# Performance work log

Measured on AMD Instinct MI355X. Metric: run time of the kernel, lower is better.

## Reference

```python
import jax, jax.numpy as jnp
import numpy as np

N_CELLS = 50000
HID = 64
DEG = 16
K_NODES = 4  # nodes per cell; cell i owns nodes [4i, 4i+4)
SP = 3


def setup_inputs() -> dict:
    key = jax.random.key(0)
    ks = jax.random.split(key, 12)
    s = 1.0 / np.sqrt(HID)
    inp = {
        'features': jax.random.normal(ks[0], (N_CELLS, HID), jnp.float32),
        'positions': jax.random.normal(ks[1], (K_NODES * N_CELLS, SP), jnp.float32),
        'neighbors': jax.random.randint(ks[2], (N_CELLS, DEG), 0, N_CELLS, jnp.int32),
        # message MLP: Linear(2H+1 -> H), SiLU, Linear(H -> H)
        'W1': jax.random.normal(ks[3], (2 * HID + 1, HID), jnp.float32) * s,
        'b1': jnp.zeros((HID,), jnp.float32),
        'W2': jax.random.normal(ks[4], (HID, HID), jnp.float32) * s,
        'b2': jnp.zeros((HID,), jnp.float32),
        # update MLP: Linear(H + H -> H), SiLU, Linear(H -> H)
        'Wu1': jax.random.normal(ks[5], (2 * HID, HID), jnp.float32) * s,
        'bu1': jnp.zeros((HID,), jnp.float32),
        'Wu2': jax.random.normal(ks[6], (HID, HID), jnp.float32) * s,
        'bu2': jnp.zeros((HID,), jnp.float32),
    }
    return inp


def reference(features, positions, neighbors, W1, b1, W2, b2, Wu1, bu1, Wu2, bu2):
    N, H = features.shape
    # centroid of each cell's owned nodes (cell i -> nodes [K*i, K*i+K))
    cent = positions.reshape(N, K_NODES, SP).mean(axis=1)          # [N, sp]
    fj = features[neighbors]                                       # [N, D, H]
    cj = cent[neighbors]                                           # [N, D, sp]
    # centroid-distance geometric invariant per (cell, neighbor) pair
    geom = jnp.linalg.norm(cent[:, None, :] - cj, axis=-1, keepdims=True)  # [N, D, 1]
    fi = jnp.broadcast_to(features[:, None, :], fj.shape)          # [N, D, H]
    x = jnp.concatenate([fi, fj, geom], axis=-1)                   # [N, D, 2H+1]
    h = jax.nn.silu(x @ W1 + b1) @ W2 + b2                         # [N, D, H]
    msg = h.mean(axis=1)                                           # mean over neighbors
    u = jnp.concatenate([features, msg], axis=-1)                  # [N, 2H]
    upd = jax.nn.silu(u @ Wu1 + bu1) @ Wu2 + bu2
    updated_features = features + upd
    return updated_features, positions
```

## Files before the change

kernel.cpp:

```cpp
#include <hip/hip_runtime.h>


#define DEG 16

typedef __attribute__((ext_vector_type(8))) short short8;
typedef __attribute__((ext_vector_type(4))) float f32x4;
typedef uint2 uint2_a __attribute__((may_alias));
typedef uint4 uint4_a __attribute__((may_alias));

union HbRd { uint4_a u; short8 s; };
union Frag { short8 s; uint4 u; };

__device__ __forceinline__ unsigned f2bf(float f) {
  unsigned u = __float_as_uint(f);
  return (u + 0x7FFFu + ((u >> 16) & 1u)) >> 16;
}
__device__ __forceinline__ float bf2f(unsigned bits16) {
  return __uint_as_float(bits16 << 16);
}
__device__ __forceinline__ float silu(float h) {
  return h / (1.f + __expf(-h));
}

__global__ __launch_bounds__(256) void aux_kernel(
    const float* __restrict__ pos,
    const float* __restrict__ W1, const float* __restrict__ W2,
    const float* __restrict__ Wu1, const float* __restrict__ Wu2,
    float* __restrict__ outpos,
    unsigned short* __restrict__ w1pq, unsigned short* __restrict__ w2t,
    unsigned short* __restrict__ wu1t, unsigned short* __restrict__ wu2b)
{
  int t = blockIdx.x * 256 + threadIdx.x;
  if (t < 150000) {
    ((float4*)outpos)[t] = ((const float4*)pos)[t];
  } else if (t < 174576) {
    const int r = t - 150000;
    if (r < 8192) {
      const int j = r & 7, l = (r >> 3) & 15, q = (r >> 7) & 3;
      const int f = r >> 9, kk = f & 1, mt = f >> 1;
      const int k = kk * 32 + q * 8 + j;
      const int m = mt * 16 + l;
      w1pq[r] = (unsigned short)f2bf(
          (m < 64) ? W1[k * 64 + m] : W1[(k + 64) * 64 + (m - 64)]);
    } else if (r < 12288) {
      const int s = r - 8192;
      const int j = s & 7, l = (s >> 3) & 15, q = (s >> 7) & 3;
      const int f = s >> 9, kk = f & 1, mt = f >> 1;
      const int k = kk * 32 + q * 8 + j;
      w2t[s] = (unsigned short)f2bf(W2[k * 64 + mt * 16 + l]);
    } else if (r < 20480) {
      const int s = r - 12288;
      const int j = s & 7, l = (s >> 3) & 15, q = (s >> 7) & 3;
      const int f = s >> 9, kk = f & 3, mt = f >> 2;
      const int k = kk * 32 + q * 8 + j;
      wu1t[s] = (unsigned short)f2bf(Wu1[k * 64 + mt * 16 + l]);
    } else {
      const int s = r - 20480;
      const int j = s & 7, l = (s >> 3) & 15, q = (s >> 7) & 3;
      const int f = s >> 9, kk = f & 1, nt = f >> 1;
      const int k = kk * 32 + q * 8 + j;
      wu2b[s] = (unsigned short)f2bf(Wu2[k * 64 + nt * 16 + l]);
    }
  }
}

__global__ __launch_bounds__(256) void prep_pq_kernel(
    const float* __restrict__ feat, const float* __restrict__ pos,
    const unsigned short* __restrict__ w1pq,
    unsigned short* __restrict__ featb, float* __restrict__ cent4,
    unsigned short* __restrict__ Pb, unsigned short* __restrict__ Qb)
{
  const int lane = threadIdx.x & 63;
  const int wid  = threadIdx.x >> 6;
  const int quad = lane >> 4;
  const int l15  = lane & 15;

  const int tile = blockIdx.x * 4 + wid;
  const bool act = (tile < 3125);
  const int  tt  = act ? tile : 3124;
  const int  cr  = tt * 16 + l15;

  short8 xf[2];
  #pragma unroll
  for (int kk = 0; kk < 2; ++kk) {
    const float4 f0 = *(const float4*)(feat + cr * 64 + kk * 32 + quad * 8);
    const float4 f1 = *(const float4*)(feat + cr * 64 + kk * 32 + quad * 8 + 4);
    Frag v;
    v.s[0] = (short)f2bf(f0.x); v.s[1] = (short)f2bf(f0.y);
    v.s[2] = (short)f2bf(f0.z); v.s[3] = (short)f2bf(f0.w);
    v.s[4] = (short)f2bf(f1.x); v.s[5] = (short)f2bf(f1.y);
    v.s[6] = (short)f2bf(f1.z); v.s[7] = (short)f2bf(f1.w);
    xf[kk] = v.s;
    if (act) *(uint4*)(featb + cr * 64 + kk * 32 + quad * 8) = v.u;
  }

  if (act && lane < 16) {
    const float4* pp = (const float4*)(pos + 12 * cr);
    const float4 a = pp[0], b = pp[1], c = pp[2];
    float4 o;
    o.x = (a.x + a.w + b.z + c.y) * 0.25f;
    o.y = (a.y + b.x + b.w + c.z) * 0.25f;
    o.z = (a.z + b.y + c.x + c.w) * 0.25f;
    o.w = 0.f;
    ((float4*)cent4)[cr] = o;
  }

  short8 wf[8][2];
  #pragma unroll
  for (int mt = 0; mt < 8; ++mt)
    #pragma unroll
    for (int kk = 0; kk < 2; ++kk)
      wf[mt][kk] = *(const short8*)(w1pq + (((mt * 2 + kk) * 4 + quad) << 7) + l15 * 8);

  f32x4 acc[8] = {};
  #pragma unroll
  for (int kk = 0; kk < 2; ++kk)
    #pragma unroll
    for (int mt = 0; mt < 8; ++mt)
      acc[mt] = __builtin_amdgcn_mfma_f32_16x16x32_bf16(wf[mt][kk], xf[kk], acc[mt], 0, 0, 0);

  if (act) {
    #pragma unroll
    for (int mt = 0; mt < 8; ++mt) {
      uint2 pk;
      pk.x = f2bf(acc[mt][0]) | (f2bf(acc[mt][1]) << 16);
      pk.y = f2bf(acc[mt][2]) | (f2bf(acc[mt][3]) << 16);
      unsigned short* dst = (mt < 4)
          ? Pb + cr * 64 + mt * 16 + quad * 4
          : Qb + cr * 64 + (mt - 4) * 16 + quad * 4;
      *(uint2*)dst = pk;
    }
  }
}

__global__ __launch_bounds__(256) void gather_kernel(
    const unsigned short* __restrict__ Pb,
    const unsigned short* __restrict__ Qb,
    const float4* __restrict__ cent4,
    const int* __restrict__ nbr,
    const float* __restrict__ b1, const float* __restrict__ W1,
    unsigned short* __restrict__ sB)
{
  const int lane = threadIdx.x & 63;
  const int wid  = threadIdx.x >> 6;
  const int quad = lane >> 4;
  const int l15  = lane & 15;
  const int c4   = l15 * 4;

  const f32x4 b1c = *(const f32x4*)(b1 + c4);
  const f32x4 wlc = *(const f32x4*)(W1 + 8192 + c4);

  for (int c = blockIdx.x * 4 + wid; c < 50000; c += 12500) {
    int nj = 0; float g = 0.f;
    if (lane < 16) {
      nj = nbr[c * DEG + lane];
      const float4 ci = cent4[c];
      const float4 cj = cent4[nj];
      const float dx = ci.x - cj.x, dy = ci.y - cj.y, dz = ci.z - cj.z;
      g = sqrtf(dx * dx + dy * dy + dz * dz);
    }

    const uint2 pv = *(const uint2*)(Pb + c * 64 + c4);
    float pc[4];
    pc[0] = bf2f(pv.x & 0xFFFFu) + b1c[0];
    pc[1] = bf2f(pv.x >> 16)     + b1c[1];
    pc[2] = bf2f(pv.y & 0xFFFFu) + b1c[2];
    pc[3] = bf2f(pv.y >> 16)     + b1c[3];

    float acc0 = 0.f, acc1 = 0.f, acc2 = 0.f, acc3 = 0.f;
    #pragma unroll
    for (int dd = 0; dd < 4; ++dd) {
      const int   d  = quad + dd * 4;
      const float gd = __shfl(g, d);
      const int   nd = __shfl(nj, d);
      const uint2 qv = *(const uint2*)(Qb + nd * 64 + c4);
      acc0 += silu(pc[0] + bf2f(qv.x & 0xFFFFu) + gd * wlc[0]);
      acc1 += silu(pc[1] + bf2f(qv.x >> 16)     + gd * wlc[1]);
      acc2 += silu(pc[2] + bf2f(qv.y & 0xFFFFu) + gd * wlc[2]);
      acc3 += silu(pc[3] + bf2f(qv.y >> 16)     + gd * wlc[3]);
    }
    acc0 += __shfl_xor(acc0, 16); acc0 += __shfl_xor(acc0, 32);
    acc1 += __shfl_xor(acc1, 16); acc1 += __shfl_xor(acc1, 32);
    acc2 += __shfl_xor(acc2, 16); acc2 += __shfl_xor(acc2, 32);
    acc3 += __shfl_xor(acc3, 16); acc3 += __shfl_xor(acc3, 32);

    if (lane < 16) {
      uint2 pk;
      pk.x = f2bf(acc0 * 0.0625f) | (f2bf(acc1 * 0.0625f) << 16);
      pk.y = f2bf(acc2 * 0.0625f) | (f2bf(acc3 * 0.0625f) << 16);
      *(uint2*)(sB + c * 64 + c4) = pk;
    }
  }
}

__global__ __launch_bounds__(256) void tail_kernel(
    const unsigned short* __restrict__ featb,
    const unsigned short* __restrict__ sB,
    const float* __restrict__ feat,
    const unsigned short* __restrict__ w2t,
    const unsigned short* __restrict__ wu1t,
    const unsigned short* __restrict__ wu2b,
    const float* __restrict__ b2, const float* __restrict__ bu1,
    const float* __restrict__ bu2,
    float* __restrict__ outf)
{
  __shared__ uint4 smem[4 * 288];
  const int lane = threadIdx.x & 63;
  const int wid  = threadIdx.x >> 6;
  const int quad = lane >> 4;
  const int l15  = lane & 15;
  char* Msg = (char*)(smem + wid * 288);
  char* Hb  = Msg + 2304;

  short8 w2f[4][2];
  #pragma unroll
  for (int mt = 0; mt < 4; ++mt)
    #pragma unroll
    for (int kk = 0; kk < 2; ++kk)
      w2f[mt][kk] = *(const short8*)(w2t + (((mt * 2 + kk) * 4 + quad) << 7) + l15 * 8);
  short8 wu1f[4][4];
  #pragma unroll
  for (int mt = 0; mt < 4; ++mt)
    #pragma unroll
    for (int kk = 0; kk < 4; ++kk)
      wu1f[mt][kk] = *(const short8*)(wu1t + (((mt * 4 + kk) * 4 + quad) << 7) + l15 * 8);
  short8 wu2f[4][2];
  #pragma unroll
  for (int nt = 0; nt < 4; ++nt)
    #pragma unroll
    for (int kk = 0; kk < 2; ++kk)
      wu2f[nt][kk] = *(const short8*)(wu2b + (((nt * 2 + kk) * 4 + quad) << 7) + l15 * 8);

  f32x4 b2f[4], bu1f[4];
  #pragma unroll
  for (int mt = 0; mt < 4; ++mt) {
    b2f[mt]  = *(const f32x4*)(b2  + mt * 16 + quad * 4);
    bu1f[mt] = *(const f32x4*)(bu1 + mt * 16 + quad * 4);
  }
  float bu2v[4];
  #pragma unroll
  for (int nt = 0; nt < 4; ++nt) bu2v[nt] = bu2[nt * 16 + l15];

  const int tile = blockIdx.x * 4 + wid;
  const bool act = (tile < 3125);
  const int  tt  = act ? tile : 3124;
  const int  cr  = tt * 16 + l15;

  f32x4 accm[4] = {};
  #pragma unroll
  for (int kk = 0; kk < 2; ++kk) {
    const short8 bf = *(const short8*)(sB + cr * 64 + kk * 32 + quad * 8);
    #pragma unroll
    for (int mt = 0; mt < 4; ++mt)
      accm[mt] = __builtin_amdgcn_mfma_f32_16x16x32_bf16(w2f[mt][kk], bf, accm[mt], 0, 0, 0);
  }
  #pragma unroll
  for (int mt = 0; mt < 4; ++mt) {
    uint2 pk;
    pk.x = f2bf(accm[mt][0] + b2f[mt][0]) | (f2bf(accm[mt][1] + b2f[mt][1]) << 16);
    pk.y = f2bf(accm[mt][2] + b2f[mt][2]) | (f2bf(accm[mt][3] + b2f[mt][3]) << 16);
    *(uint2_a*)(Msg + l15 * 144 + mt * 32 + quad * 8) = pk;
  }
  __threadfence_block();

  f32x4 accu[4] = {};
  #pragma unroll
  for (int kk = 0; kk < 4; ++kk) {
    short8 bf;
    if (kk < 2) {
      bf = *(const short8*)(featb + cr * 64 + kk * 32 + quad * 8);
    } else {
      HbRd t; t.u = *(const uint4_a*)(Msg + l15 * 144 + (kk - 2) * 64 + quad * 16);
      bf = t.s;
    }
    #pragma unroll
    for (int mt = 0; mt < 4; ++mt)
      accu[mt] = __builtin_amdgcn_mfma_f32_16x16x32_bf16(wu1f[mt][kk], bf, accu[mt], 0, 0, 0);
  }
  #pragma unroll
  for (int mt = 0; mt < 4; ++mt) {
    float sv[4];
    #pragma unroll
    for (int rg = 0; rg < 4; ++rg)
      sv[rg] = silu(accu[mt][rg] + bu1f[mt][rg]);
    uint2 pk;
    pk.x = f2bf(sv[0]) | (f2bf(sv[1]) << 16);
    pk.y = f2bf(sv[2]) | (f2bf(sv[3]) << 16);
    *(uint2_a*)(Hb + l15 * 144 + mt * 32 + quad * 8) = pk;
  }
  __threadfence_block();

  f32x4 acc2[4] = {};
  #pragma unroll
  for (int kk = 0; kk < 2; ++kk) {
    HbRd t; t.u = *(const uint4_a*)(Hb + l15 * 144 + kk * 64 + quad * 16);
    const short8 af = t.s;
    #pragma unroll
    for (int nt = 0; nt < 4; ++nt)
      acc2[nt] = __builtin_amdgcn_mfma_f32_16x16x32_bf16(af, wu2f[nt][kk], acc2[nt], 0, 0, 0);
  }
  if (act) {
    #pragma unroll
    for (int nt = 0; nt < 4; ++nt)
      #pragma unroll
      for (int rg = 0; rg < 4; ++rg) {
        const int row = tt * 16 + quad * 4 + rg;
        const int col = nt * 16 + l15;
        outf[row * 64 + col] = feat[row * 64 + col] + acc2[nt][rg] + bu2v[nt];
      }
  }
}

extern "C" void kernel_launch(void* const* d_in, const int* in_sizes, int n_in,
                              void* d_out, int out_size, void* d_ws, size_t ws_size,
                              hipStream_t stream)
{
  const float* feat = (const float*)d_in[0];
  const float* pos  = (const float*)d_in[1];
  const int*   nbr  = (const int*)d_in[2];
  const float* W1   = (const float*)d_in[3];
  const float* b1   = (const float*)d_in[4];
  const float* W2   = (const float*)d_in[5];
  const float* b2   = (const float*)d_in[6];
  const float* Wu1  = (const float*)d_in[7];
  const float* bu1  = (const float*)d_in[8];
  const float* Wu2  = (const float*)d_in[9];
  const float* bu2  = (const float*)d_in[10];
  float* out = (float*)d_out;

  unsigned short* featb = (unsigned short*)d_ws;
  unsigned short* Pb    = (unsigned short*)((char*)d_ws + 6400000);
  unsigned short* Qb    = (unsigned short*)((char*)d_ws + 12800000);
  unsigned short* sB    = (unsigned short*)((char*)d_ws + 19200000);
  float*          cent4 = (float*)((char*)d_ws + 25600000);
  unsigned short* w1pq  = (unsigned short*)((char*)d_ws + 26400000);
  unsigned short* w2t   = (unsigned short*)((char*)d_ws + 26416384);
  unsigned short* wu1t  = (unsigned short*)((char*)d_ws + 26424576);
  unsigned short* wu2b  = (unsigned short*)((char*)d_ws + 26440960);

  aux_kernel<<<682, 256, 0, stream>>>(pos, W1, W2, Wu1, Wu2, out + 3200000,
                                      w1pq, w2t, wu1t, wu2b);
  prep_pq_kernel<<<782, 256, 0, stream>>>(feat, pos, w1pq, featb, cent4, Pb, Qb);
  gather_kernel<<<3125, 256, 0, stream>>>(Pb, Qb, (const float4*)cent4, nbr,
                                          b1, W1, sB);
  tail_kernel<<<782, 256, 0, stream>>>(featb, sB, feat, w2t, wu1t, wu2b,
                                       b2, bu1, bu2, out);
}
```

Baseline: 143.2 us.

## Remap gather kernel to one neighbor per lane group with 16 channels per lane

The gather kernel's lane mapping changes: each wave still handles one cell, but each lane now takes one neighbor and 16 channels. Previously each lane covered 4 channels and looped over 4 neighbors. The grid-stride loop is dropped in favor of 12500 blocks, one cell per wave. Loads become 16-byte Q/P reads with fully parallel gathers, which should raise memory-level parallelism. In exchange the cross-neighbor reduction grows to 4 shuffle stages over 16 values each, which adds shuffle traffic and register pressure.

```diff
diff --git a/kernel.cpp b/kernel.cpp
--- a/kernel.cpp
+++ b/kernel.cpp
@@ -20,6 +20,12 @@
 }
 __device__ __forceinline__ float silu(float h) {
   return h / (1.f + __expf(-h));
+}
+__device__ __forceinline__ void unpack8(const uint4 v, float* o) {
+  o[0] = bf2f(v.x & 0xFFFFu); o[1] = bf2f(v.x >> 16);
+  o[2] = bf2f(v.y & 0xFFFFu); o[3] = bf2f(v.y >> 16);
+  o[4] = bf2f(v.z & 0xFFFFu); o[5] = bf2f(v.z >> 16);
+  o[6] = bf2f(v.w & 0xFFFFu); o[7] = bf2f(v.w >> 16);
 }
 
 __global__ __launch_bounds__(256) void aux_kernel(
@@ -143,53 +149,56 @@
 {
   const int lane = threadIdx.x & 63;
   const int wid  = threadIdx.x >> 6;
-  const int quad = lane >> 4;
-  const int l15  = lane & 15;
-  const int c4   = l15 * 4;
-
-  const f32x4 b1c = *(const f32x4*)(b1 + c4);
-  const f32x4 wlc = *(const f32x4*)(W1 + 8192 + c4);
-
-  for (int c = blockIdx.x * 4 + wid; c < 50000; c += 12500) {
-    int nj = 0; float g = 0.f;
-    if (lane < 16) {
-      nj = nbr[c * DEG + lane];
-      const float4 ci = cent4[c];
-      const float4 cj = cent4[nj];
-      const float dx = ci.x - cj.x, dy = ci.y - cj.y, dz = ci.z - cj.z;
-      g = sqrtf(dx * dx + dy * dy + dz * dz);
-    }
-
-    const uint2 pv = *(const uint2*)(Pb + c * 64 + c4);
-    float pc[4];
-    pc[0] = bf2f(pv.x & 0xFFFFu) + b1c[0];
-    pc[1] = bf2f(pv.x >> 16)     + b1c[1];
-    pc[2] = bf2f(pv.y & 0xFFFFu) + b1c[2];
-    pc[3] = bf2f(pv.y >> 16)     + b1c[3];
-
-    float acc0 = 0.f, acc1 = 0.f, acc2 = 0.f, acc3 = 0.f;
-    #pragma unroll
-    for (int dd = 0; dd < 4; ++dd) {
-      const int   d  = quad + dd * 4;
-      const float gd = __shfl(g, d);
-      const int   nd = __shfl(nj, d);
-      const uint2 qv = *(const uint2*)(Qb + nd * 64 + c4);
-      acc0 += silu(pc[0] + bf2f(qv.x & 0xFFFFu) + gd * wlc[0]);
-      acc1 += silu(pc[1] + bf2f(qv.x >> 16)     + gd * wlc[1]);
-      acc2 += silu(pc[2] + bf2f(qv.y & 0xFFFFu) + gd * wlc[2]);
-      acc3 += silu(pc[3] + bf2f(qv.y >> 16)     + gd * wlc[3]);
-    }
-    acc0 += __shfl_xor(acc0, 16); acc0 += __shfl_xor(acc0, 32);
-    acc1 += __shfl_xor(acc1, 16); acc1 += __shfl_xor(acc1, 32);
-    acc2 += __shfl_xor(acc2, 16); acc2 += __shfl_xor(acc2, 32);
-    acc3 += __shfl_xor(acc3, 16); acc3 += __shfl_xor(acc3, 32);
-
-    if (lane < 16) {
-      uint2 pk;
-      pk.x = f2bf(acc0 * 0.0625f) | (f2bf(acc1 * 0.0625f) << 16);
-      pk.y = f2bf(acc2 * 0.0625f) | (f2bf(acc3 * 0.0625f) << 16);
-      *(uint2*)(sB + c * 64 + c4) = pk;
-    }
+  const int d    = lane >> 2;
+  const int cg   = lane & 3;
+  const int cb   = cg * 16;
+  const int c    = blockIdx.x * 4 + wid;
+
+  const int nd = nbr[c * DEG + d];
+
+  const float4 ci = cent4[c];
+  const float4 cj = cent4[nd];
+  const float dx = ci.x - cj.x, dy = ci.y - cj.y, dz = ci.z - cj.z;
+  const float g = sqrtf(dx * dx + dy * dy + dz * dz);
+
+  float pc[16], wl[16];
+  unpack8(*(const uint4*)(Pb + c * 64 + cb),     pc);
+  unpack8(*(const uint4*)(Pb + c * 64 + cb + 8), pc + 8);
+  #pragma unroll
+  for (int k = 0; k < 16; k += 4) {
+    const float4 bv = *(const float4*)(b1 + cb + k);
+    const float4 wv = *(const float4*)(W1 + 8192 + cb + k);
+    pc[k] += bv.x; pc[k+1] += bv.y; pc[k+2] += bv.z; pc[k+3] += bv.w;
+    wl[k] = wv.x; wl[k+1] = wv.y; wl[k+2] = wv.z; wl[k+3] = wv.w;
+  }
+
+  float qf[16];
+  unpack8(*(const uint4*)(Qb + nd * 64 + cb),     qf);
+  unpack8(*(const uint4*)(Qb + nd * 64 + cb + 8), qf + 8);
+
+  float acc[16];
+  #pragma unroll
+  for (int k = 0; k < 16; ++k)
+    acc[k] = silu(pc[k] + qf[k] + g * wl[k]);
+
+  #pragma unroll
+  for (int s = 4; s <= 32; s <<= 1)
+    #pragma unroll
+    for (int k = 0; k < 16; ++k)
+      acc[k] += __shfl_xor(acc[k], s);
+
+  if (lane < 4) {
+    uint4 o0, o1;
+    o0.x = f2bf(acc[0]*0.0625f)  | (f2bf(acc[1]*0.0625f)  << 16);
+    o0.y = f2bf(acc[2]*0.0625f)  | (f2bf(acc[3]*0.0625f)  << 16);
+    o0.z = f2bf(acc[4]*0.0625f)  | (f2bf(acc[5]*0.0625f)  << 16);
+    o0.w = f2bf(acc[6]*0.0625f)  | (f2bf(acc[7]*0.0625f)  << 16);
+    o1.x = f2bf(acc[8]*0.0625f)  | (f2bf(acc[9]*0.0625f)  << 16);
+    o1.y = f2bf(acc[10]*0.0625f) | (f2bf(acc[11]*0.0625f) << 16);
+    o1.z = f2bf(acc[12]*0.0625f) | (f2bf(acc[13]*0.0625f) << 16);
+    o1.w = f2bf(acc[14]*0.0625f) | (f2bf(acc[15]*0.0625f) << 16);
+    *(uint4*)(sB + c * 64 + cb)     = o0;
+    *(uint4*)(sB + c * 64 + cb + 8) = o1;
   }
 }
 
@@ -341,8 +350,8 @@
   aux_kernel<<<682, 256, 0, stream>>>(pos, W1, W2, Wu1, Wu2, out + 3200000,
                                       w1pq, w2t, wu1t, wu2b);
   prep_pq_kernel<<<782, 256, 0, stream>>>(feat, pos, w1pq, featb, cent4, Pb, Qb);
-  gather_kernel<<<3125, 256, 0, stream>>>(Pb, Qb, (const float4*)cent4, nbr,
-                                          b1, W1, sB);
+  gather_kernel<<<12500, 256, 0, stream>>>(Pb, Qb, (const float4*)cent4, nbr,
+                                           b1, W1, sB);
   tail_kernel<<<782, 256, 0, stream>>>(featb, sB, feat, w2t, wu1t, wu2b,
                                        b2, bu1, bu2, out);
 }
```

Measured after the change: 147.0 us. +2.7%, slower.

## Remap gather kernel to one channel per lane with readlane neighbor broadcast

Applied to the files above, without the earlier changes.

The gather kernel now assigns one hidden channel per lane and iterates over all 16 neighbors in-lane, broadcasting neighbor index and distance with readlane. This removes the cross-lane xor-shuffle reduction and the grid-stride loop, launching one wave per cell. It trades wider 8-byte loads for more 2-byte loads, and has every lane compute the centroid distance redundantly.

```diff
diff --git a/kernel.cpp b/kernel.cpp
--- a/kernel.cpp
+++ b/kernel.cpp
@@ -143,54 +143,29 @@
 {
   const int lane = threadIdx.x & 63;
   const int wid  = threadIdx.x >> 6;
-  const int quad = lane >> 4;
-  const int l15  = lane & 15;
-  const int c4   = l15 * 4;
-
-  const f32x4 b1c = *(const f32x4*)(b1 + c4);
-  const f32x4 wlc = *(const f32x4*)(W1 + 8192 + c4);
-
-  for (int c = blockIdx.x * 4 + wid; c < 50000; c += 12500) {
-    int nj = 0; float g = 0.f;
-    if (lane < 16) {
-      nj = nbr[c * DEG + lane];
-      const float4 ci = cent4[c];
-      const float4 cj = cent4[nj];
-      const float dx = ci.x - cj.x, dy = ci.y - cj.y, dz = ci.z - cj.z;
-      g = sqrtf(dx * dx + dy * dy + dz * dz);
-    }
-
-    const uint2 pv = *(const uint2*)(Pb + c * 64 + c4);
-    float pc[4];
-    pc[0] = bf2f(pv.x & 0xFFFFu) + b1c[0];
-    pc[1] = bf2f(pv.x >> 16)     + b1c[1];
-    pc[2] = bf2f(pv.y & 0xFFFFu) + b1c[2];
-    pc[3] = bf2f(pv.y >> 16)     + b1c[3];
-
-    float acc0 = 0.f, acc1 = 0.f, acc2 = 0.f, acc3 = 0.f;
-    #pragma unroll
-    for (int dd = 0; dd < 4; ++dd) {
-      const int   d  = quad + dd * 4;
-      const float gd = __shfl(g, d);
-      const int   nd = __shfl(nj, d);
-      const uint2 qv = *(const uint2*)(Qb + nd * 64 + c4);
-      acc0 += silu(pc[0] + bf2f(qv.x & 0xFFFFu) + gd * wlc[0]);
-      acc1 += silu(pc[1] + bf2f(qv.x >> 16)     + gd * wlc[1]);
-      acc2 += silu(pc[2] + bf2f(qv.y & 0xFFFFu) + gd * wlc[2]);
-      acc3 += silu(pc[3] + bf2f(qv.y >> 16)     + gd * wlc[3]);
-    }
-    acc0 += __shfl_xor(acc0, 16); acc0 += __shfl_xor(acc0, 32);
-    acc1 += __shfl_xor(acc1, 16); acc1 += __shfl_xor(acc1, 32);
-    acc2 += __shfl_xor(acc2, 16); acc2 += __shfl_xor(acc2, 32);
-    acc3 += __shfl_xor(acc3, 16); acc3 += __shfl_xor(acc3, 32);
-
-    if (lane < 16) {
-      uint2 pk;
-      pk.x = f2bf(acc0 * 0.0625f) | (f2bf(acc1 * 0.0625f) << 16);
-      pk.y = f2bf(acc2 * 0.0625f) | (f2bf(acc3 * 0.0625f) << 16);
-      *(uint2*)(sB + c * 64 + c4) = pk;
-    }
-  }
+  const int c    = blockIdx.x * 4 + wid;
+
+  const int nj = nbr[c * DEG + (lane & 15)];
+
+  const float4 ci = cent4[c];
+  const float4 cj = cent4[nj];
+  const float dx = ci.x - cj.x, dy = ci.y - cj.y, dz = ci.z - cj.z;
+  const float g = sqrtf(dx * dx + dy * dy + dz * dz);
+
+  const float pcb = bf2f(Pb[c * 64 + lane]) + b1[lane];
+  const float wl  = W1[8192 + lane];
+
+  float acc = 0.f;
+  #pragma unroll
+  for (int d = 0; d < DEG; ++d) {
+    const int   nd = __builtin_amdgcn_readlane(nj, d);
+    const float gd = __uint_as_float(
+        __builtin_amdgcn_readlane((int)__float_as_uint(g), d));
+    const float qv = bf2f(Qb[nd * 64 + lane]);
+    acc += silu(pcb + qv + gd * wl);
+  }
+
+  sB[c * 64 + lane] = (unsigned short)f2bf(acc * 0.0625f);
 }
 
 __global__ __launch_bounds__(256) void tail_kernel(
@@ -341,8 +316,8 @@
   aux_kernel<<<682, 256, 0, stream>>>(pos, W1, W2, Wu1, Wu2, out + 3200000,
                                       w1pq, w2t, wu1t, wu2b);
   prep_pq_kernel<<<782, 256, 0, stream>>>(feat, pos, w1pq, featb, cent4, Pb, Qb);
-  gather_kernel<<<3125, 256, 0, stream>>>(Pb, Qb, (const float4*)cent4, nbr,
-                                          b1, W1, sB);
+  gather_kernel<<<12500, 256, 0, stream>>>(Pb, Qb, (const float4*)cent4, nbr,
+                                           b1, W1, sB);
   tail_kernel<<<782, 256, 0, stream>>>(featb, sB, feat, w2t, wu1t, wu2b,
                                        b2, bu1, bu2, out);
 }
```

Measured after the change: 141.4 us. Within noise of the previous version (-1.2%).
